# Optimization experiments

Measured on AMD Instinct MI355X. Metric: run time of the kernel, lower is better.

The kernel has to match this reference:

```python
import jax, jax.numpy as jnp
import numpy as np

B, L, D = 4, 2048, 1024
EV = 64            # event_embed_dim
EXPAND = 2
DI = EXPAND * D    # d_inner = 2048
N = 16             # d_state
K = 4              # d_conv
DT_RANK = (D + 15) // 16  # 64
EPS = 1e-5


def setup_inputs() -> dict:
    key = jax.random.key(0)
    ks = jax.random.split(key, 16)
    g = lambda k, shape, s=0.02: (jax.random.normal(k, shape, dtype=jnp.float32) * s)
    return {
        "x": jax.random.normal(ks[0], (B, L, D), dtype=jnp.float32),
        "event_emb": jax.random.normal(ks[1], (B, L, EV), dtype=jnp.float32),
        "W_in": g(ks[2], (D + EV, D)),
        "b_in": jnp.zeros((D,), jnp.float32),
        "ln_g": jnp.ones((D,), jnp.float32),
        "ln_b": jnp.zeros((D,), jnp.float32),
        "in_proj_w": g(ks[3], (D, 2 * DI)),
        "conv_w": g(ks[4], (DI, K), 0.1),
        "conv_b": jnp.zeros((DI,), jnp.float32),
        "x_proj_w": g(ks[5], (DI, DT_RANK + 2 * N)),
        "dt_proj_w": g(ks[6], (DT_RANK, DI), 0.1),
        "dt_proj_b": jnp.full((DI,), -4.6, jnp.float32),  # ~softplus^-1(0.01)
        "A_log": jnp.log(jnp.broadcast_to(jnp.arange(1, N + 1, dtype=jnp.float32), (DI, N))),
        "D_param": jnp.ones((DI,), jnp.float32),
        "out_proj_w": g(ks[7], (DI, D)),
    }


def _mamba_block(x, event_emb, W_in, b_in, ln_g, ln_b, in_proj_w, conv_w, conv_b,
                 x_proj_w, dt_proj_w, dt_proj_b, A_log, D_param, out_proj_w):
    d_conv = conv_w.shape[1]
    n_state = A_log.shape[1]
    dt_rank = dt_proj_w.shape[0]
    Lx = x.shape[1]

    aug = jnp.concatenate([x, event_emb], axis=-1) @ W_in + b_in   # [B,L,D]
    residual = aug
    mu = aug.mean(-1, keepdims=True)
    var = jnp.mean((aug - mu) ** 2, axis=-1, keepdims=True)
    h = (aug - mu) * jax.lax.rsqrt(var + EPS) * ln_g + ln_b

    xz = h @ in_proj_w                                             # [B,L,2*DI]
    xh, z = jnp.split(xz, 2, axis=-1)

    # causal depthwise conv1d (width d_conv)
    xp = jnp.pad(xh, ((0, 0), (d_conv - 1, 0), (0, 0)))
    xc = conv_b
    for k in range(d_conv):
        xc = xc + conv_w[:, k] * xp[:, k:k + Lx, :]
    xc = jax.nn.silu(xc)                                           # [B,L,DI]

    dbl = xc @ x_proj_w                                            # [B,L,dt_rank+2N]
    dt, Bm, Cm = jnp.split(dbl, [dt_rank, dt_rank + n_state], axis=-1)
    dt = jax.nn.softplus(dt @ dt_proj_w + dt_proj_b)               # [B,L,DI]
    A = -jnp.exp(A_log)                                            # [DI,N]

    def step(hst, inp):
        dt_t, B_t, C_t, u_t = inp                                  # [B,DI],[B,N],[B,N],[B,DI]
        dA = jnp.exp(dt_t[:, :, None] * A)                         # [B,DI,N]
        dBu = (dt_t * u_t)[:, :, None] * B_t[:, None, :]           # [B,DI,N]
        hst = dA * hst + dBu
        y_t = jnp.einsum('bdn,bn->bd', hst, C_t)
        return hst, y_t

    h0 = jnp.zeros((xc.shape[0], xc.shape[2], n_state), xc.dtype)
    xs = (dt.transpose(1, 0, 2), Bm.transpose(1, 0, 2),
          Cm.transpose(1, 0, 2), xc.transpose(1, 0, 2))
    _, ys = jax.lax.scan(step, h0, xs)                             # [L,B,DI]
    y = ys.transpose(1, 0, 2) + D_param * xc
    y = y * jax.nn.silu(z)
    return residual + y @ out_proj_w                               # [B,L,D]


def reference(x, event_emb, W_in, b_in, ln_g, ln_b, in_proj_w, conv_w, conv_b,
              x_proj_w, dt_proj_w, dt_proj_b, A_log, D_param, out_proj_w):
    return _mamba_block(x, event_emb, W_in, b_in, ln_g, ln_b, in_proj_w, conv_w,
                        conv_b, x_proj_w, dt_proj_w, dt_proj_b, A_log, D_param,
                        out_proj_w)
```

## Files before the change

kernel.cpp:

```cpp
#include <hip/hip_runtime.h>
#include <cstdint>
#include <cstddef>

#define DEV __device__ __forceinline__

typedef __bf16 bf16x8 __attribute__((ext_vector_type(8)));
typedef float f32x4 __attribute__((ext_vector_type(4)));

DEV unsigned short f2bf(float f) {
  unsigned u = __builtin_bit_cast(unsigned, f);
  u += 0x7fffu + ((u >> 16) & 1u);
  return (unsigned short)(u >> 16);
}
DEV float bf2f(unsigned short h) {
  return __builtin_bit_cast(float, (unsigned)h << 16);
}

__global__ __launch_bounds__(256)
void k_concat(const float* __restrict__ x, const float* __restrict__ ev,
              unsigned short* __restrict__ Aaug) {
  int col4 = blockIdx.x * 256 + threadIdx.x;
  if (col4 >= 288) return;
  size_t row = blockIdx.y;
  float4 v = make_float4(0.f, 0.f, 0.f, 0.f);
  if (col4 < 256)      v = reinterpret_cast<const float4*>(x + row * 1024)[col4];
  else if (col4 < 272) v = reinterpret_cast<const float4*>(ev + row * 64)[col4 - 256];
  ushort4 o; o.x = f2bf(v.x); o.y = f2bf(v.y); o.z = f2bf(v.z); o.w = f2bf(v.w);
  reinterpret_cast<ushort4*>(Aaug + row * 1152)[col4] = o;
}

__global__ void k_transpose(const float* __restrict__ in, unsigned short* __restrict__ out,
                            int R, int C, int Rout, int Cout) {
  __shared__ float tile[32][33];
  int c0 = blockIdx.x * 32, r0 = blockIdx.y * 32;
  int tx = threadIdx.x, ty = threadIdx.y;
#pragma unroll
  for (int i = 0; i < 4; ++i) {
    int r = r0 + ty + i * 8, c = c0 + tx;
    tile[ty + i * 8][tx] = (r < R && c < C) ? in[(size_t)r * C + c] : 0.f;
  }
  __syncthreads();
#pragma unroll
  for (int i = 0; i < 4; ++i) {
    int c = c0 + ty + i * 8, r = r0 + tx;
    if (c < Cout && r < Rout) out[(size_t)c * Rout + r] = f2bf(tile[tx][ty + i * 8]);
  }
}

template <int BN, int EPI>
__global__ __launch_bounds__(512, 2)
void k_gemm8(const unsigned short* __restrict__ A, const unsigned short* __restrict__ Bt,
             int N, int NT, int lda, int ldb,
             float* __restrict__ outF, unsigned short* __restrict__ outB1,
             unsigned short* __restrict__ outB2,
             const float* __restrict__ bias, const float* __restrict__ resid) {
  static_assert(BN == 128 || BN == 256, "");
  constexpr int NF = BN / 64;
  constexpr int NHF = NF / 2;
  constexpr int BLOADS = BN / 128;
  constexpr int ATILE = 256 * 64;
  constexpr int BTILE = BN * 64;
  constexpr int BUFSZ = ATILE + BTILE;
  __shared__ unsigned short lds[2 * BUFSZ];

  const int tid = threadIdx.x;
  const int lane = tid & 63, w = tid >> 6;
  const int wm = w >> 2, wn = w & 3;
  const int frow = lane & 15, fk = lane >> 4;

  const int nbx = gridDim.x;
  const int nwg = nbx * gridDim.y;
  const int orig = blockIdx.y * nbx + blockIdx.x;
  const int swz = (orig & 7) * (nwg >> 3) + (orig >> 3);
  const int brow = swz / nbx, bcol = swz % nbx;
  const size_t row0 = (size_t)brow * 256, col0 = (size_t)bcol * BN;

  f32x4 acc[8][NF];
#pragma unroll
  for (int i = 0; i < 8; ++i)
#pragma unroll
    for (int j = 0; j < NF; ++j) acc[i][j] = f32x4{0.f, 0.f, 0.f, 0.f};

  bf16x8 afr[4][2], bq0[NHF][2], bq1[NHF][2];

  auto stageA = [&](int p, int tau, int half) {
    unsigned short* dst = lds + p * BUFSZ + half * 4096 + w * 512;
#pragma unroll
    for (int l = 0; l < 2; ++l) {
      int row = l * 128 + half * 64 + (tid >> 3);
      int g = (tid & 7) ^ (row & 7);
      const unsigned short* src = A + (row0 + row) * lda + tau * 64 + g * 8;
      __builtin_amdgcn_global_load_lds(src, dst + l * 8192, 16, 0, 0);
    }
  };
  auto stageB = [&](int p, int tau, int half) {
    unsigned short* dst = lds + p * BUFSZ + ATILE + half * (BTILE / 2) + w * 512;
#pragma unroll
    for (int l = 0; l < BLOADS; ++l) {
      int row = half * (BN / 2) + l * 64 + (tid >> 3);
      int g = (tid & 7) ^ (row & 7);
      const unsigned short* src = Bt + (col0 + row) * ldb + tau * 64 + g * 8;
      __builtin_amdgcn_global_load_lds(src, dst + l * 4096, 16, 0, 0);
    }
  };
  auto ldA = [&](int p, int mh) {
#pragma unroll
    for (int mi = 0; mi < 4; ++mi)
#pragma unroll
      for (int kb = 0; kb < 2; ++kb) {
        int rr = wm * 128 + mh * 64 + mi * 16 + frow;
        int gk = kb * 4 + fk;
        afr[mi][kb] = *reinterpret_cast<const bf16x8*>(
            lds + p * BUFSZ + rr * 64 + ((gk ^ (rr & 7)) * 8));
      }
  };
  auto ldB = [&](int p, int nh, bf16x8 (&bq)[NHF][2]) {
#pragma unroll
    for (int ni = 0; ni < NHF; ++ni)
#pragma unroll
      for (int kb = 0; kb < 2; ++kb) {
        int cc = wn * (BN / 4) + nh * (BN / 8) + ni * 16 + frow;
        int gk = kb * 4 + fk;
        bq[ni][kb] = *reinterpret_cast<const bf16x8*>(
            lds + p * BUFSZ + ATILE + cc * 64 + ((gk ^ (cc & 7)) * 8));
      }
  };

#define MMAQ(MH, NH, BQ)                                                          \
  do {                                                                            \
    __builtin_amdgcn_s_setprio(1);                                                \
    _Pragma("unroll") for (int mi = 0; mi < 4; ++mi)                              \
        _Pragma("unroll") for (int ni = 0; ni < NHF; ++ni)                        \
            _Pragma("unroll") for (int kb = 0; kb < 2; ++kb)                      \
                acc[(MH)*4 + mi][(NH)*NHF + ni] =                                 \
                    __builtin_amdgcn_mfma_f32_16x16x32_bf16(                      \
                        afr[mi][kb], BQ[ni][kb], acc[(MH)*4 + mi][(NH)*NHF + ni], \
                        0, 0, 0);                                                 \
    __builtin_amdgcn_s_setprio(0);                                                \
  } while (0)

#define BARC  __builtin_amdgcn_s_barrier()
#define SBAR  __builtin_amdgcn_sched_barrier(0)
#define EBAR  do { __builtin_amdgcn_s_barrier(); __builtin_amdgcn_sched_barrier(0); } while (0)
#define VMCNT_WAIT                                                     \
  do {                                                                 \
    if constexpr (BN == 256)                                           \
      asm volatile("s_waitcnt vmcnt(6)" ::: "memory");                 \
    else                                                               \
      asm volatile("s_waitcnt vmcnt(4)" ::: "memory");                 \
  } while (0)

  stageA(0, 0, 0); stageB(0, 0, 0); stageB(0, 0, 1); stageA(0, 0, 1);
  SBAR;
  stageA(1, 1, 0); stageB(1, 1, 0); stageB(1, 1, 1);
  VMCNT_WAIT;
  BARC; SBAR;

  const int niter = NT >> 1;
  for (int it = 0; it < niter; ++it) {
    int t = 2 * it;
    int t1s = t + 1;
    int t2s = (t + 2 < NT) ? t + 2 : NT - 1;
    int t3s = (t + 3 < NT) ? t + 3 : NT - 1;
    ldA(0, 0); ldB(0, 0, bq0);
    stageA(1, t1s, 1);
    BARC; MMAQ(0, 0, bq0); EBAR;
    ldB(0, 1, bq1);
    stageA(0, t2s, 0);
    BARC; MMAQ(0, 1, bq1); EBAR;
    ldA(0, 1);
    stageB(0, t2s, 0);
    BARC; MMAQ(1, 1, bq1); EBAR;
    stageB(0, t2s, 1);
    BARC; MMAQ(1, 0, bq0); VMCNT_WAIT; EBAR;
    ldA(1, 0); ldB(1, 0, bq0);
    stageA(0, t2s, 1);
    BARC; MMAQ(0, 0, bq0); EBAR;
    ldB(1, 1, bq1);
    stageA(1, t3s, 0);
    BARC; MMAQ(0, 1, bq1); EBAR;
    ldA(1, 1);
    stageB(1, t3s, 0);
    BARC; MMAQ(1, 1, bq1); EBAR;
    stageB(1, t3s, 1);
    BARC; MMAQ(1, 0, bq0); VMCNT_WAIT; EBAR;
  }

#pragma unroll
  for (int q = 0; q < 8; ++q) {
#pragma unroll
    for (int j = 0; j < NF; ++j) {
#pragma unroll
      for (int r = 0; r < 4; ++r) {
        size_t row = row0 + wm * 128 + q * 16 + fk * 4 + r;
        size_t col = col0 + wn * (BN / 4) + j * 16 + frow;
        float v = acc[q][j][r];
        if constexpr (EPI == 0) {
          outF[row * N + col] = v + bias[col];
        } else if constexpr (EPI == 1) {
          int hn = N >> 1;
          if ((int)col < hn) outB1[row * hn + col] = f2bf(v);
          else               outB2[row * hn + (col - hn)] = f2bf(v);
        } else {
          outF[row * N + col] = resid[row * N + col] + v;
        }
      }
    }
  }
#undef MMAQ
#undef BARC
#undef SBAR
#undef EBAR
#undef VMCNT_WAIT
}

template <int EPI>
__global__ __launch_bounds__(256)
void k_gemm(const unsigned short* __restrict__ A, const unsigned short* __restrict__ Bt,
            int N, int K, int lda, int ldb,
            unsigned short* __restrict__ outB1, const float* __restrict__ bias) {
  __shared__ alignas(16) unsigned short sA[128 * 64];
  __shared__ alignas(16) unsigned short sB[128 * 64];
  int tid = threadIdx.x;
  int lane = tid & 63, w = tid >> 6;
  int nbx = gridDim.x;
  int nwg = nbx * gridDim.y;
  int orig = blockIdx.y * nbx + blockIdx.x;
  int swz = (orig & 7) * (nwg >> 3) + (orig >> 3);
  int brow = swz / nbx, bcol = swz % nbx;
  size_t row0 = (size_t)brow * 128, col0 = (size_t)bcol * 128;

  int lrow_s = tid >> 3;
  int g_s = tid & 7;
  int wrow = (w >> 1) * 64, wcol = (w & 1) * 64;
  int frow = lane & 15, fk = lane >> 4;
  f32x4 acc[4][4] = {};

  for (int kt = 0; kt < K; kt += 64) {
    __syncthreads();
#pragma unroll
    for (int r = 0; r < 4; ++r) {
      int lr = r * 32 + lrow_s;
      int gs = g_s ^ (lr & 7);
      const unsigned short* srcA = A + (size_t)(row0 + lr) * lda + kt + gs * 8;
      const unsigned short* srcB = Bt + (size_t)(col0 + lr) * ldb + kt + gs * 8;
      unsigned short* dstA = sA + (r * 32 + w * 8) * 64;
      unsigned short* dstB = sB + (r * 32 + w * 8) * 64;
      __builtin_amdgcn_global_load_lds(srcA, dstA, 16, 0, 0);
      __builtin_amdgcn_global_load_lds(srcB, dstB, 16, 0, 0);
    }
    __syncthreads();
#pragma unroll
    for (int kw = 0; kw < 2; ++kw) {
      bf16x8 af[4], bfr[4];
      int gk = kw * 4 + fk;
#pragma unroll
      for (int mi = 0; mi < 4; ++mi) {
        int rr = wrow + mi * 16 + frow;
        af[mi] = *reinterpret_cast<const bf16x8*>(sA + rr * 64 + ((gk ^ (rr & 7)) * 8));
      }
#pragma unroll
      for (int ni = 0; ni < 4; ++ni) {
        int rr = wcol + ni * 16 + frow;
        bfr[ni] = *reinterpret_cast<const bf16x8*>(sB + rr * 64 + ((gk ^ (rr & 7)) * 8));
      }
#pragma unroll
      for (int mi = 0; mi < 4; ++mi)
#pragma unroll
        for (int ni = 0; ni < 4; ++ni)
          acc[mi][ni] = __builtin_amdgcn_mfma_f32_16x16x32_bf16(af[mi], bfr[ni], acc[mi][ni], 0, 0, 0);
    }
  }

#pragma unroll
  for (int mi = 0; mi < 4; ++mi) {
#pragma unroll
    for (int ni = 0; ni < 4; ++ni) {
#pragma unroll
      for (int r = 0; r < 4; ++r) {
        size_t row = row0 + wrow + mi * 16 + fk * 4 + r;
        size_t col = col0 + wcol + ni * 16 + frow;
        float v = acc[mi][ni][r];
        if constexpr (EPI == 2) {
          outB1[row * N + col] = f2bf(v);
        } else {
          float xx = v + bias[col];
          float sp = (xx > 15.f) ? xx : __logf(1.f + __expf(xx));
          outB1[row * N + col] = f2bf(sp);
        }
      }
    }
  }
}

__global__ __launch_bounds__(256)
void k_ln(const float* __restrict__ aug, const float* __restrict__ gam,
          const float* __restrict__ bet, unsigned short* __restrict__ h) {
  int tid = threadIdx.x;
  size_t row = blockIdx.x;
  float4 v = reinterpret_cast<const float4*>(aug + row * 1024)[tid];
  float s = v.x + v.y + v.z + v.w;
  float ss = v.x * v.x + v.y * v.y + v.z * v.z + v.w * v.w;
#pragma unroll
  for (int m = 32; m >= 1; m >>= 1) {
    s += __shfl_xor(s, m, 64);
    ss += __shfl_xor(ss, m, 64);
  }
  __shared__ float rb[8];
  if ((tid & 63) == 0) { rb[tid >> 6] = s; rb[4 + (tid >> 6)] = ss; }
  __syncthreads();
  float ts = rb[0] + rb[1] + rb[2] + rb[3];
  float tss = rb[4] + rb[5] + rb[6] + rb[7];
  float mu = ts * (1.f / 1024.f);
  float var = tss * (1.f / 1024.f) - mu * mu;
  float rs = rsqrtf(var + 1e-5f);
  float4 gv = reinterpret_cast<const float4*>(gam)[tid];
  float4 bv = reinterpret_cast<const float4*>(bet)[tid];
  ushort4 o;
  o.x = f2bf((v.x - mu) * rs * gv.x + bv.x);
  o.y = f2bf((v.y - mu) * rs * gv.y + bv.y);
  o.z = f2bf((v.z - mu) * rs * gv.z + bv.z);
  o.w = f2bf((v.w - mu) * rs * gv.w + bv.w);
  reinterpret_cast<ushort4*>(h + row * 1024)[tid] = o;
}

__global__ __launch_bounds__(256)
void k_conv(const unsigned short* __restrict__ xh, const float* __restrict__ cw,
            const float* __restrict__ cb, unsigned short* __restrict__ xc) {
  int d = blockIdx.x * 256 + threadIdx.x;
  int t = blockIdx.y, b = blockIdx.z;
  size_t rowb = (size_t)b * 2048;
  float acc = cb[d];
#pragma unroll
  for (int k = 0; k < 4; ++k) {
    int tt = t - 3 + k;
    if (tt >= 0) acc += cw[d * 4 + k] * bf2f(xh[(rowb + tt) * 2048 + d]);
  }
  float sg = 1.f / (1.f + __expf(-acc));
  xc[(rowb + t) * 2048 + d] = f2bf(acc * sg);
}

template <bool FINAL>
__global__ __launch_bounds__(256)
void k_scan(const unsigned short* __restrict__ dt, const unsigned short* __restrict__ xc,
            const unsigned short* __restrict__ dbl, const float* __restrict__ A_log,
            float* __restrict__ S, float* __restrict__ SD,
            const float* __restrict__ Hin, const float* __restrict__ Dp,
            const unsigned short* __restrict__ z, unsigned short* __restrict__ yg) {
  int d = blockIdx.x * 256 + threadIdx.x;
  int b = blockIdx.y, c = blockIdx.z;
  int t0 = c * 32;
  size_t hoff = (((size_t)c * 4 + b) * 2048 + d) * 16;
  float An[16], h[16];
  bool fast = true;
#pragma unroll
  for (int n = 0; n < 16; ++n) {
    An[n] = -__expf(A_log[((size_t)d << 4) + n]);
    fast = fast && (__builtin_fabsf(An[n] + (float)(n + 1)) < 1e-4f);
    h[n] = FINAL ? Hin[hoff + n] : 0.f;
  }
  float Dv = FINAL ? Dp[d] : 0.f;
  float dts = 0.f;
  __shared__ float sBC[32][32];
  if (threadIdx.x < 128) {
    int s = threadIdx.x >> 2, j8 = (threadIdx.x & 3) * 8;
    size_t rowg = (size_t)b * 2048 + t0 + s;
    uint4 raw = *reinterpret_cast<const uint4*>(dbl + rowg * 128 + 64 + j8);
    unsigned rr4[4] = {raw.x, raw.y, raw.z, raw.w};
#pragma unroll
    for (int q = 0; q < 4; ++q) {
      sBC[s][j8 + 2 * q]     = bf2f((unsigned short)(rr4[q] & 0xffffu));
      sBC[s][j8 + 2 * q + 1] = bf2f((unsigned short)(rr4[q] >> 16));
    }
  }
  __syncthreads();

  if (fast) {
    for (int si = 0; si < 32; ++si) {
      size_t rr = ((size_t)b * 2048 + t0 + si) * 2048 + d;
      float dtv = bf2f(dt[rr]);
      float uv = bf2f(xc[rr]);
      float dtu = dtv * uv;
      float y = 0.f;
      if constexpr (!FINAL) dts += dtv;
      float e1 = __expf(-dtv);
      float a = e1;
#pragma unroll
      for (int n = 0; n < 16; ++n) {
        h[n] = a * h[n] + dtu * sBC[si][n];
        if constexpr (FINAL) y += h[n] * sBC[si][16 + n];
        a *= e1;
      }
      if constexpr (FINAL) {
        float zv = bf2f(z[rr]);
        float sig = 1.f / (1.f + __expf(-zv));
        yg[rr] = f2bf((y + Dv * uv) * (zv * sig));
      }
    }
  } else {
    for (int si = 0; si < 32; ++si) {
      size_t rr = ((size_t)b * 2048 + t0 + si) * 2048 + d;
      float dtv = bf2f(dt[rr]);
      float uv = bf2f(xc[rr]);
      float dtu = dtv * uv;
      float y = 0.f;
      if constexpr (!FINAL) dts += dtv;
#pragma unroll
      for (int n = 0; n < 16; ++n) {
        float a = __expf(dtv * An[n]);
        h[n] = a * h[n] + dtu * sBC[si][n];
        if constexpr (FINAL) y += h[n] * sBC[si][16 + n];
      }
      if constexpr (FINAL) {
        float zv = bf2f(z[rr]);
        float sig = 1.f / (1.f + __expf(-zv));
        yg[rr] = f2bf((y + Dv * uv) * (zv * sig));
      }
    }
  }
  if constexpr (!FINAL) {
#pragma unroll
    for (int n = 0; n < 16; ++n) S[hoff + n] = h[n];
    SD[((size_t)c * 4 + b) * 2048 + d] = dts;
  }
}

__global__ __launch_bounds__(256)
void k_scanB(float* __restrict__ S, const float* __restrict__ SD,
             const float* __restrict__ A_log) {
  int id = blockIdx.x * 256 + threadIdx.x;
  int n = id & 15, d = (id >> 4) & 2047, b = id >> 15;
  float An = -__expf(A_log[((size_t)d << 4) + n]);
  float h = 0.f;
  for (int c = 0; c < 64; ++c) {
    size_t sdo = ((size_t)c * 4 + b) * 2048 + d;
    size_t o = sdo * 16 + n;
    float s = S[o];
    float p = __expf(An * SD[sdo]);
    S[o] = h;
    h = s + p * h;
  }
}

extern "C" void kernel_launch(void* const* d_in, const int* in_sizes, int n_in,
                              void* d_out, int out_size, void* d_ws, size_t ws_size,
                              hipStream_t stream) {
  const float* x       = (const float*)d_in[0];
  const float* ev      = (const float*)d_in[1];
  const float* W_in    = (const float*)d_in[2];
  const float* b_in    = (const float*)d_in[3];
  const float* ln_g    = (const float*)d_in[4];
  const float* ln_b    = (const float*)d_in[5];
  const float* in_proj = (const float*)d_in[6];
  const float* conv_w  = (const float*)d_in[7];
  const float* conv_b  = (const float*)d_in[8];
  const float* x_proj  = (const float*)d_in[9];
  const float* dt_proj = (const float*)d_in[10];
  const float* dt_b    = (const float*)d_in[11];
  const float* A_log   = (const float*)d_in[12];
  const float* D_par   = (const float*)d_in[13];
  const float* out_w   = (const float*)d_in[14];
  float* out = (float*)d_out;

  char* ws = (char*)d_ws;
  size_t off = 0;
  auto alloc = [&](size_t bytes) {
    char* p = ws + off;
    off = (off + bytes + 255) & ~(size_t)255;
    return p;
  };
  float* aug            = (float*)alloc(8192ull * 1024 * 4);
  unsigned short* dtfb  = (unsigned short*)alloc(8192ull * 2048 * 2);
  unsigned short* Aaug  = (unsigned short*)alloc(8192ull * 1152 * 2);
  unsigned short* WinT  = (unsigned short*)alloc(1024ull * 1152 * 2);
  unsigned short* ipT   = (unsigned short*)alloc(4096ull * 1024 * 2);
  unsigned short* xpT   = (unsigned short*)alloc(128ull * 2048 * 2);
  unsigned short* dpT   = (unsigned short*)alloc(2048ull * 64 * 2);
  unsigned short* opT   = (unsigned short*)alloc(1024ull * 2048 * 2);
  unsigned short* xh    = (unsigned short*)alloc(8192ull * 2048 * 2);
  unsigned short* zb    = (unsigned short*)alloc(8192ull * 2048 * 2);
  unsigned short* xcb   = (unsigned short*)alloc(8192ull * 2048 * 2);
  unsigned short* dbl   = (unsigned short*)alloc(8192ull * 128 * 2);
  float* Sb = (float*)alloc(64ull * 4 * 2048 * 16 * 4);
  float* SD = (float*)alloc(64ull * 4 * 2048 * 4);
  unsigned short* hb = Aaug;
  unsigned short* yg = xh;

  k_concat<<<dim3(2, 8192), 256, 0, stream>>>(x, ev, Aaug);
  k_transpose<<<dim3(32, 36), dim3(32, 8), 0, stream>>>(W_in, WinT, 1088, 1024, 1152, 1024);
  k_transpose<<<dim3(128, 32), dim3(32, 8), 0, stream>>>(in_proj, ipT, 1024, 4096, 1024, 4096);
  k_transpose<<<dim3(4, 64), dim3(32, 8), 0, stream>>>(x_proj, xpT, 2048, 96, 2048, 128);
  k_transpose<<<dim3(64, 2), dim3(32, 8), 0, stream>>>(dt_proj, dpT, 64, 2048, 64, 2048);
  k_transpose<<<dim3(32, 64), dim3(32, 8), 0, stream>>>(out_w, opT, 2048, 1024, 2048, 1024);

  k_gemm8<128, 0><<<dim3(8, 32), 512, 0, stream>>>(Aaug, WinT, 1024, 18, 1152, 1152,
                                                   aug, nullptr, nullptr, b_in, nullptr);
  k_ln<<<dim3(8192), 256, 0, stream>>>(aug, ln_g, ln_b, hb);
  k_gemm8<256, 1><<<dim3(16, 32), 512, 0, stream>>>(hb, ipT, 4096, 16, 1024, 1024,
                                                    nullptr, xh, zb, nullptr, nullptr);
  k_conv<<<dim3(8, 2048, 4), 256, 0, stream>>>(xh, conv_w, conv_b, xcb);
  k_gemm<2><<<dim3(1, 64), 256, 0, stream>>>(xcb, xpT, 128, 2048, 2048, 2048, dbl, nullptr);
  k_gemm<3><<<dim3(16, 64), 256, 0, stream>>>(dbl, dpT, 2048, 64, 128, 64, dtfb, dt_b);
  k_scan<false><<<dim3(8, 4, 64), 256, 0, stream>>>(dtfb, xcb, dbl, A_log, Sb, SD,
                                                    nullptr, nullptr, nullptr, nullptr);
  k_scanB<<<dim3(512), 256, 0, stream>>>(Sb, SD, A_log);
  k_scan<true><<<dim3(8, 4, 64), 256, 0, stream>>>(dtfb, xcb, dbl, A_log, nullptr, nullptr,
                                                   Sb, D_par, zb, yg);
  k_gemm8<128, 4><<<dim3(8, 32), 512, 0, stream>>>(yg, opT, 1024, 32, 2048, 2048,
                                                   out, nullptr, nullptr, nullptr, aug);
}
```

Before: 412.9 us.

## Switch GEMMs to 32x32 MFMA, add multi-tile persistent blocks, split scan exponent chain

The GEMM kernel moves from 16x16x32 to 32x32x16 bf16 MFMA fragments with f32x16 accumulators, which changes the LDS fragment loads and the epilogue layout. A new MT template parameter lets one workgroup process two M tiles back to back without draining the pipeline, with an in-loop epilogue that writes results and clears the accumulators. The in_proj GEMM uses MT=2 on half the grid. Separately, the scan's serial a*=e1 power chain is replaced by precomputed powers to shorten the dependency chain. Together these aim to raise MFMA throughput and ILP, at the cost of register pressure and a different output access pattern.

```diff
diff --git a/kernel.cpp b/kernel.cpp
--- a/kernel.cpp
+++ b/kernel.cpp
@@ -6,6 +6,7 @@
 
 typedef __bf16 bf16x8 __attribute__((ext_vector_type(8)));
 typedef float f32x4 __attribute__((ext_vector_type(4)));
+typedef float f32x16 __attribute__((ext_vector_type(16)));
 
 DEV unsigned short f2bf(float f) {
   unsigned u = __builtin_bit_cast(unsigned, f);
@@ -47,7 +48,7 @@
   }
 }
 
-template <int BN, int EPI>
+template <int BN, int MT, int EPI>
 __global__ __launch_bounds__(512, 2)
 void k_gemm8(const unsigned short* __restrict__ A, const unsigned short* __restrict__ Bt,
              int N, int NT, int lda, int ldb,
@@ -55,8 +56,8 @@
              unsigned short* __restrict__ outB2,
              const float* __restrict__ bias, const float* __restrict__ resid) {
   static_assert(BN == 128 || BN == 256, "");
-  constexpr int NF = BN / 64;
-  constexpr int NHF = NF / 2;
+  constexpr int NC = BN / 128;
+  constexpr int BQN = (BN == 256) ? 4 : 2;
   constexpr int BLOADS = BN / 128;
   constexpr int ATILE = 256 * 64;
   constexpr int BTILE = BN * 64;
@@ -66,77 +67,85 @@
   const int tid = threadIdx.x;
   const int lane = tid & 63, w = tid >> 6;
   const int wm = w >> 2, wn = w & 3;
-  const int frow = lane & 15, fk = lane >> 4;
+  const int ln31 = lane & 31, lk = lane >> 5;
 
   const int nbx = gridDim.x;
   const int nwg = nbx * gridDim.y;
   const int orig = blockIdx.y * nbx + blockIdx.x;
   const int swz = (orig & 7) * (nwg >> 3) + (orig >> 3);
   const int brow = swz / nbx, bcol = swz % nbx;
-  const size_t row0 = (size_t)brow * 256, col0 = (size_t)bcol * BN;
-
-  f32x4 acc[8][NF];
-#pragma unroll
-  for (int i = 0; i < 8; ++i)
-#pragma unroll
-    for (int j = 0; j < NF; ++j) acc[i][j] = f32x4{0.f, 0.f, 0.f, 0.f};
-
-  bf16x8 afr[4][2], bq0[NHF][2], bq1[NHF][2];
+  const size_t rowBase = (size_t)brow * (256 * MT);
+  const size_t col0 = (size_t)bcol * BN;
+  const int TT = MT * NT;
+
+  f32x16 acc[4][NC];
+#pragma unroll
+  for (int i = 0; i < 4; ++i)
+#pragma unroll
+    for (int j = 0; j < NC; ++j)
+#pragma unroll
+      for (int r = 0; r < 16; ++r) acc[i][j][r] = 0.f;
+
+  bf16x8 afr[2][4], bq0[BQN], bq1[BQN];
 
   auto stageA = [&](int p, int tau, int half) {
+    int tm = (MT > 1 && tau >= NT) ? 1 : 0;
+    int kt = tau - tm * NT;
     unsigned short* dst = lds + p * BUFSZ + half * 4096 + w * 512;
 #pragma unroll
     for (int l = 0; l < 2; ++l) {
       int row = l * 128 + half * 64 + (tid >> 3);
       int g = (tid & 7) ^ (row & 7);
-      const unsigned short* src = A + (row0 + row) * lda + tau * 64 + g * 8;
+      const unsigned short* src = A + (rowBase + tm * 256 + row) * lda + kt * 64 + g * 8;
       __builtin_amdgcn_global_load_lds(src, dst + l * 8192, 16, 0, 0);
     }
   };
   auto stageB = [&](int p, int tau, int half) {
+    int tm = (MT > 1 && tau >= NT) ? 1 : 0;
+    int kt = tau - tm * NT;
     unsigned short* dst = lds + p * BUFSZ + ATILE + half * (BTILE / 2) + w * 512;
 #pragma unroll
     for (int l = 0; l < BLOADS; ++l) {
       int row = half * (BN / 2) + l * 64 + (tid >> 3);
       int g = (tid & 7) ^ (row & 7);
-      const unsigned short* src = Bt + (col0 + row) * ldb + tau * 64 + g * 8;
+      const unsigned short* src = Bt + (col0 + row) * ldb + kt * 64 + g * 8;
       __builtin_amdgcn_global_load_lds(src, dst + l * 4096, 16, 0, 0);
     }
   };
   auto ldA = [&](int p, int mh) {
 #pragma unroll
-    for (int mi = 0; mi < 4; ++mi)
-#pragma unroll
-      for (int kb = 0; kb < 2; ++kb) {
-        int rr = wm * 128 + mh * 64 + mi * 16 + frow;
-        int gk = kb * 4 + fk;
-        afr[mi][kb] = *reinterpret_cast<const bf16x8*>(
+    for (int mf = 0; mf < 2; ++mf)
+#pragma unroll
+      for (int ks = 0; ks < 4; ++ks) {
+        int rr = wm * 128 + mh * 64 + mf * 32 + ln31;
+        int gk = ks * 2 + lk;
+        afr[mf][ks] = *reinterpret_cast<const bf16x8*>(
             lds + p * BUFSZ + rr * 64 + ((gk ^ (rr & 7)) * 8));
       }
   };
-  auto ldB = [&](int p, int nh, bf16x8 (&bq)[NHF][2]) {
-#pragma unroll
-    for (int ni = 0; ni < NHF; ++ni)
-#pragma unroll
-      for (int kb = 0; kb < 2; ++kb) {
-        int cc = wn * (BN / 4) + nh * (BN / 8) + ni * 16 + frow;
-        int gk = kb * 4 + fk;
-        bq[ni][kb] = *reinterpret_cast<const bf16x8*>(
-            lds + p * BUFSZ + ATILE + cc * 64 + ((gk ^ (cc & 7)) * 8));
-      }
+  auto ldB = [&](int p, int nh, bf16x8 (&bq)[BQN]) {
+#pragma unroll
+    for (int q = 0; q < BQN; ++q) {
+      int nf = (BN == 256) ? nh : 0;
+      int ks = (BN == 256) ? q : (nh * 2 + q);
+      int cc = wn * (BN / 4) + nf * 32 + ln31;
+      int gk = ks * 2 + lk;
+      bq[q] = *reinterpret_cast<const bf16x8*>(
+          lds + p * BUFSZ + ATILE + cc * 64 + ((gk ^ (cc & 7)) * 8));
+    }
   };
 
-#define MMAQ(MH, NH, BQ)                                                          \
-  do {                                                                            \
-    __builtin_amdgcn_s_setprio(1);                                                \
-    _Pragma("unroll") for (int mi = 0; mi < 4; ++mi)                              \
-        _Pragma("unroll") for (int ni = 0; ni < NHF; ++ni)                        \
-            _Pragma("unroll") for (int kb = 0; kb < 2; ++kb)                      \
-                acc[(MH)*4 + mi][(NH)*NHF + ni] =                                 \
-                    __builtin_amdgcn_mfma_f32_16x16x32_bf16(                      \
-                        afr[mi][kb], BQ[ni][kb], acc[(MH)*4 + mi][(NH)*NHF + ni], \
-                        0, 0, 0);                                                 \
-    __builtin_amdgcn_s_setprio(0);                                                \
+#define MMAQ(MH, NH, BQ)                                                           \
+  do {                                                                             \
+    __builtin_amdgcn_s_setprio(1);                                                 \
+    _Pragma("unroll") for (int mf = 0; mf < 2; ++mf)                               \
+        _Pragma("unroll") for (int q = 0; q < BQN; ++q) {                          \
+      constexpr int nfi = (BN == 256) ? (NH) : 0;                                  \
+      acc[(MH)*2 + mf][nfi] = __builtin_amdgcn_mfma_f32_32x32x16_bf16(             \
+          afr[mf][(BN == 256) ? q : ((NH)*2 + q)], BQ[q], acc[(MH)*2 + mf][nfi],   \
+          0, 0, 0);                                                                \
+    }                                                                              \
+    __builtin_amdgcn_s_setprio(0);                                                 \
   } while (0)
 
 #define BARC  __builtin_amdgcn_s_barrier()
@@ -150,18 +159,45 @@
       asm volatile("s_waitcnt vmcnt(4)" ::: "memory");                 \
   } while (0)
 
+  auto epilogue = [&](int tm) {
+    size_t tRow0 = rowBase + (size_t)tm * 256;
+#pragma unroll
+    for (int mf = 0; mf < 4; ++mf) {
+#pragma unroll
+      for (int nf = 0; nf < NC; ++nf) {
+#pragma unroll
+        for (int r = 0; r < 16; ++r) {
+          size_t row = tRow0 + wm * 128 + mf * 32 + (r & 3) + 8 * (r >> 2) + 4 * lk;
+          size_t col = col0 + wn * (BN / 4) + nf * 32 + ln31;
+          float v = acc[mf][nf][r];
+          if constexpr (EPI == 0) {
+            outF[row * N + col] = v + bias[col];
+          } else if constexpr (EPI == 1) {
+            int hn = N >> 1;
+            if ((int)col < hn) outB1[row * hn + col] = f2bf(v);
+            else               outB2[row * hn + (col - hn)] = f2bf(v);
+          } else {
+            outF[row * N + col] = resid[row * N + col] + v;
+          }
+          acc[mf][nf][r] = 0.f;
+        }
+      }
+    }
+  };
+
   stageA(0, 0, 0); stageB(0, 0, 0); stageB(0, 0, 1); stageA(0, 0, 1);
   SBAR;
   stageA(1, 1, 0); stageB(1, 1, 0); stageB(1, 1, 1);
   VMCNT_WAIT;
   BARC; SBAR;
 
-  const int niter = NT >> 1;
+  int kcnt = 0, tmdone = 0;
+  const int niter = TT >> 1;
   for (int it = 0; it < niter; ++it) {
     int t = 2 * it;
     int t1s = t + 1;
-    int t2s = (t + 2 < NT) ? t + 2 : NT - 1;
-    int t3s = (t + 3 < NT) ? t + 3 : NT - 1;
+    int t2s = (t + 2 < TT) ? t + 2 : TT - 1;
+    int t3s = (t + 3 < TT) ? t + 3 : TT - 1;
     ldA(0, 0); ldB(0, 0, bq0);
     stageA(1, t1s, 1);
     BARC; MMAQ(0, 0, bq0); EBAR;
@@ -184,28 +220,8 @@
     BARC; MMAQ(1, 1, bq1); EBAR;
     stageB(1, t3s, 1);
     BARC; MMAQ(1, 0, bq0); VMCNT_WAIT; EBAR;
-  }
-
-#pragma unroll
-  for (int q = 0; q < 8; ++q) {
-#pragma unroll
-    for (int j = 0; j < NF; ++j) {
-#pragma unroll
-      for (int r = 0; r < 4; ++r) {
-        size_t row = row0 + wm * 128 + q * 16 + fk * 4 + r;
-        size_t col = col0 + wn * (BN / 4) + j * 16 + frow;
-        float v = acc[q][j][r];
-        if constexpr (EPI == 0) {
-          outF[row * N + col] = v + bias[col];
-        } else if constexpr (EPI == 1) {
-          int hn = N >> 1;
-          if ((int)col < hn) outB1[row * hn + col] = f2bf(v);
-          else               outB2[row * hn + (col - hn)] = f2bf(v);
-        } else {
-          outF[row * N + col] = resid[row * N + col] + v;
-        }
-      }
-    }
+    kcnt += 2;
+    if (kcnt == NT) { epilogue(tmdone); ++tmdone; kcnt = 0; }
   }
 #undef MMAQ
 #undef BARC
@@ -384,12 +400,16 @@
       float y = 0.f;
       if constexpr (!FINAL) dts += dtv;
       float e1 = __expf(-dtv);
-      float a = e1;
+      float e2 = e1 * e1;
+      float e3 = e2 * e1, e4 = e2 * e2;
+      float e8 = e4 * e4, e12 = e8 * e4;
+      float base[4] = {e1, e2, e3, e4};
+      float mul[4] = {1.f, e4, e8, e12};
 #pragma unroll
       for (int n = 0; n < 16; ++n) {
+        float a = base[n & 3] * mul[n >> 2];
         h[n] = a * h[n] + dtu * sBC[si][n];
         if constexpr (FINAL) y += h[n] * sBC[si][16 + n];
-        a *= e1;
       }
       if constexpr (FINAL) {
         float zv = bf2f(z[rr]);
@@ -493,11 +513,11 @@
   k_transpose<<<dim3(64, 2), dim3(32, 8), 0, stream>>>(dt_proj, dpT, 64, 2048, 64, 2048);
   k_transpose<<<dim3(32, 64), dim3(32, 8), 0, stream>>>(out_w, opT, 2048, 1024, 2048, 1024);
 
-  k_gemm8<128, 0><<<dim3(8, 32), 512, 0, stream>>>(Aaug, WinT, 1024, 18, 1152, 1152,
-                                                   aug, nullptr, nullptr, b_in, nullptr);
+  k_gemm8<128, 1, 0><<<dim3(8, 32), 512, 0, stream>>>(Aaug, WinT, 1024, 18, 1152, 1152,
+                                                      aug, nullptr, nullptr, b_in, nullptr);
   k_ln<<<dim3(8192), 256, 0, stream>>>(aug, ln_g, ln_b, hb);
-  k_gemm8<256, 1><<<dim3(16, 32), 512, 0, stream>>>(hb, ipT, 4096, 16, 1024, 1024,
-                                                    nullptr, xh, zb, nullptr, nullptr);
+  k_gemm8<256, 2, 1><<<dim3(16, 16), 512, 0, stream>>>(hb, ipT, 4096, 16, 1024, 1024,
+                                                       nullptr, xh, zb, nullptr, nullptr);
   k_conv<<<dim3(8, 2048, 4), 256, 0, stream>>>(xh, conv_w, conv_b, xcb);
   k_gemm<2><<<dim3(1, 64), 256, 0, stream>>>(xcb, xpT, 128, 2048, 2048, 2048, dbl, nullptr);
   k_gemm<3><<<dim3(16, 64), 256, 0, stream>>>(dbl, dpT, 2048, 64, 128, 64, dtfb, dt_b);
@@ -506,6 +526,6 @@
   k_scanB<<<dim3(512), 256, 0, stream>>>(Sb, SD, A_log);
   k_scan<true><<<dim3(8, 4, 64), 256, 0, stream>>>(dtfb, xcb, dbl, A_log, nullptr, nullptr,
                                                    Sb, D_par, zb, yg);
-  k_gemm8<128, 4><<<dim3(8, 32), 512, 0, stream>>>(yg, opT, 1024, 32, 2048, 2048,
-                                                   out, nullptr, nullptr, nullptr, aug);
-}
+  k_gemm8<128, 1, 4><<<dim3(8, 32), 512, 0, stream>>>(yg, opT, 1024, 32, 2048, 2048,
+                                                      out, nullptr, nullptr, nullptr, aug);
+}
```

Result: slower. 474.4 us (+14.9%).

## Hoist GEMM address math, vectorize conv, break scan decay dependency chain

Applied to the files above, without the earlier changes.

The GEMM kernel now precomputes its global source offsets and swizzled LDS fragment addresses once, instead of recomputing them per stage, and relaxes launch bounds from 2 to 1 block per CU so more registers are available. The depthwise conv kernel now has each thread handle 8 channels with vector loads and stores, launched one block per row. The scan's fast path computes the decay powers from a few base products rather than a serial multiply chain, shortening the dependency chain. The risks are lower occupancy in the GEMM and higher register use in conv.

```diff
diff --git a/kernel.cpp b/kernel.cpp
--- a/kernel.cpp
+++ b/kernel.cpp
@@ -48,7 +48,7 @@
 }
 
 template <int BN, int EPI>
-__global__ __launch_bounds__(512, 2)
+__global__ __launch_bounds__(512, 1)
 void k_gemm8(const unsigned short* __restrict__ A, const unsigned short* __restrict__ Bt,
              int N, int NT, int lda, int ldb,
              float* __restrict__ outF, unsigned short* __restrict__ outB1,
@@ -83,47 +83,61 @@
 
   bf16x8 afr[4][2], bq0[NHF][2], bq1[NHF][2];
 
+  const int srow = tid >> 3;
+  const int g8 = ((tid & 7) ^ (srow & 7)) * 8;
+  const size_t offA_h0l0 = (row0 + 0 * 128 + 0 * 64 + srow) * (size_t)lda + g8;
+  const size_t offA_h0l1 = (row0 + 1 * 128 + 0 * 64 + srow) * (size_t)lda + g8;
+  const size_t offA_h1l0 = (row0 + 0 * 128 + 1 * 64 + srow) * (size_t)lda + g8;
+  const size_t offA_h1l1 = (row0 + 1 * 128 + 1 * 64 + srow) * (size_t)lda + g8;
+  const size_t offB_h0l0 = (col0 + 0 * (BN / 2) + 0 * 64 + srow) * (size_t)ldb + g8;
+  const size_t offB_h1l0 = (col0 + 1 * (BN / 2) + 0 * 64 + srow) * (size_t)ldb + g8;
+  const size_t offB_h0l1 = (BLOADS == 2) ? ((col0 + 0 * (BN / 2) + 1 * 64 + srow) * (size_t)ldb + g8) : 0;
+  const size_t offB_h1l1 = (BLOADS == 2) ? ((col0 + 1 * (BN / 2) + 1 * 64 + srow) * (size_t)ldb + g8) : 0;
+
+  char* ldsb = reinterpret_cast<char*>(lds);
+  const int fr7 = frow & 7;
+  const int slot0 = (fk ^ fr7) * 16;
+  const int slot1 = ((4 + fk) ^ fr7) * 16;
+  const int abase0 = (wm * 128 + frow) * 128 + slot0;
+  const int abase1 = (wm * 128 + frow) * 128 + slot1;
+  const int bbase0 = (wn * (BN / 4) + frow) * 128 + slot0 + ATILE * 2;
+  const int bbase1 = (wn * (BN / 4) + frow) * 128 + slot1 + ATILE * 2;
+
   auto stageA = [&](int p, int tau, int half) {
+    const size_t kadd = (size_t)tau * 64;
+    const unsigned short* s0 = A + (half ? offA_h1l0 : offA_h0l0) + kadd;
+    const unsigned short* s1 = A + (half ? offA_h1l1 : offA_h0l1) + kadd;
     unsigned short* dst = lds + p * BUFSZ + half * 4096 + w * 512;
-#pragma unroll
-    for (int l = 0; l < 2; ++l) {
-      int row = l * 128 + half * 64 + (tid >> 3);
-      int g = (tid & 7) ^ (row & 7);
-      const unsigned short* src = A + (row0 + row) * lda + tau * 64 + g * 8;
-      __builtin_amdgcn_global_load_lds(src, dst + l * 8192, 16, 0, 0);
-    }
+    __builtin_amdgcn_global_load_lds(s0, dst, 16, 0, 0);
+    __builtin_amdgcn_global_load_lds(s1, dst + 8192, 16, 0, 0);
   };
   auto stageB = [&](int p, int tau, int half) {
+    const size_t kadd = (size_t)tau * 64;
     unsigned short* dst = lds + p * BUFSZ + ATILE + half * (BTILE / 2) + w * 512;
-#pragma unroll
-    for (int l = 0; l < BLOADS; ++l) {
-      int row = half * (BN / 2) + l * 64 + (tid >> 3);
-      int g = (tid & 7) ^ (row & 7);
-      const unsigned short* src = Bt + (col0 + row) * ldb + tau * 64 + g * 8;
-      __builtin_amdgcn_global_load_lds(src, dst + l * 4096, 16, 0, 0);
+    const unsigned short* s0 = Bt + (half ? offB_h1l0 : offB_h0l0) + kadd;
+    __builtin_amdgcn_global_load_lds(s0, dst, 16, 0, 0);
+    if constexpr (BLOADS == 2) {
+      const unsigned short* s1 = Bt + (half ? offB_h1l1 : offB_h0l1) + kadd;
+      __builtin_amdgcn_global_load_lds(s1, dst + 4096, 16, 0, 0);
     }
   };
   auto ldA = [&](int p, int mh) {
-#pragma unroll
-    for (int mi = 0; mi < 4; ++mi)
-#pragma unroll
-      for (int kb = 0; kb < 2; ++kb) {
-        int rr = wm * 128 + mh * 64 + mi * 16 + frow;
-        int gk = kb * 4 + fk;
-        afr[mi][kb] = *reinterpret_cast<const bf16x8*>(
-            lds + p * BUFSZ + rr * 64 + ((gk ^ (rr & 7)) * 8));
-      }
+    const int pb = p * (BUFSZ * 2);
+#pragma unroll
+    for (int mi = 0; mi < 4; ++mi) {
+      const int off = pb + (mh * 64 + mi * 16) * 128;
+      afr[mi][0] = *reinterpret_cast<const bf16x8*>(ldsb + abase0 + off);
+      afr[mi][1] = *reinterpret_cast<const bf16x8*>(ldsb + abase1 + off);
+    }
   };
   auto ldB = [&](int p, int nh, bf16x8 (&bq)[NHF][2]) {
-#pragma unroll
-    for (int ni = 0; ni < NHF; ++ni)
-#pragma unroll
-      for (int kb = 0; kb < 2; ++kb) {
-        int cc = wn * (BN / 4) + nh * (BN / 8) + ni * 16 + frow;
-        int gk = kb * 4 + fk;
-        bq[ni][kb] = *reinterpret_cast<const bf16x8*>(
-            lds + p * BUFSZ + ATILE + cc * 64 + ((gk ^ (cc & 7)) * 8));
-      }
+    const int pb = p * (BUFSZ * 2);
+#pragma unroll
+    for (int ni = 0; ni < NHF; ++ni) {
+      const int off = pb + (nh * (BN / 8) + ni * 16) * 128;
+      bq[ni][0] = *reinterpret_cast<const bf16x8*>(ldsb + bbase0 + off);
+      bq[ni][1] = *reinterpret_cast<const bf16x8*>(ldsb + bbase1 + off);
+    }
   };
 
 #define MMAQ(MH, NH, BQ)                                                          \
@@ -327,17 +341,45 @@
 __global__ __launch_bounds__(256)
 void k_conv(const unsigned short* __restrict__ xh, const float* __restrict__ cw,
             const float* __restrict__ cb, unsigned short* __restrict__ xc) {
-  int d = blockIdx.x * 256 + threadIdx.x;
-  int t = blockIdx.y, b = blockIdx.z;
-  size_t rowb = (size_t)b * 2048;
-  float acc = cb[d];
+  size_t row = blockIdx.x;
+  int t = (int)(row & 2047);
+  size_t rowb = row - t;
+  int d = threadIdx.x * 8;
+  float acc[8];
+  {
+    float4 c0 = *reinterpret_cast<const float4*>(cb + d);
+    float4 c1 = *reinterpret_cast<const float4*>(cb + d + 4);
+    acc[0] = c0.x; acc[1] = c0.y; acc[2] = c0.z; acc[3] = c0.w;
+    acc[4] = c1.x; acc[5] = c1.y; acc[6] = c1.z; acc[7] = c1.w;
+  }
+  float wv[8][4];
+#pragma unroll
+  for (int j = 0; j < 8; ++j) {
+    float4 cj = *reinterpret_cast<const float4*>(cw + (size_t)(d + j) * 4);
+    wv[j][0] = cj.x; wv[j][1] = cj.y; wv[j][2] = cj.z; wv[j][3] = cj.w;
+  }
 #pragma unroll
   for (int k = 0; k < 4; ++k) {
     int tt = t - 3 + k;
-    if (tt >= 0) acc += cw[d * 4 + k] * bf2f(xh[(rowb + tt) * 2048 + d]);
-  }
-  float sg = 1.f / (1.f + __expf(-acc));
-  xc[(rowb + t) * 2048 + d] = f2bf(acc * sg);
+    if (tt >= 0) {
+      ushort4 va = reinterpret_cast<const ushort4*>(xh + (rowb + tt) * 2048 + d)[0];
+      ushort4 vb = reinterpret_cast<const ushort4*>(xh + (rowb + tt) * 2048 + d)[1];
+      unsigned short e[8] = {va.x, va.y, va.z, va.w, vb.x, vb.y, vb.z, vb.w};
+#pragma unroll
+      for (int j = 0; j < 8; ++j) acc[j] += wv[j][k] * bf2f(e[j]);
+    }
+  }
+  ushort4 o0, o1;
+  unsigned short* op = &o0.x;
+#pragma unroll
+  for (int j = 0; j < 8; ++j) {
+    float sg = 1.f / (1.f + __expf(-acc[j]));
+    unsigned short r = f2bf(acc[j] * sg);
+    if (j < 4) (&o0.x)[j] = r; else (&o1.x)[j - 4] = r;
+  }
+  (void)op;
+  reinterpret_cast<ushort4*>(xc + row * 2048 + d)[0] = o0;
+  reinterpret_cast<ushort4*>(xc + row * 2048 + d)[1] = o1;
 }
 
 template <bool FINAL>
@@ -384,12 +426,16 @@
       float y = 0.f;
       if constexpr (!FINAL) dts += dtv;
       float e1 = __expf(-dtv);
-      float a = e1;
+      float e2 = e1 * e1;
+      float e3 = e2 * e1, e4 = e2 * e2;
+      float e8 = e4 * e4, e12 = e8 * e4;
+      float base[4] = {e1, e2, e3, e4};
+      float mul[4] = {1.f, e4, e8, e12};
 #pragma unroll
       for (int n = 0; n < 16; ++n) {
+        float a = base[n & 3] * mul[n >> 2];
         h[n] = a * h[n] + dtu * sBC[si][n];
         if constexpr (FINAL) y += h[n] * sBC[si][16 + n];
-        a *= e1;
       }
       if constexpr (FINAL) {
         float zv = bf2f(z[rr]);
@@ -498,7 +544,7 @@
   k_ln<<<dim3(8192), 256, 0, stream>>>(aug, ln_g, ln_b, hb);
   k_gemm8<256, 1><<<dim3(16, 32), 512, 0, stream>>>(hb, ipT, 4096, 16, 1024, 1024,
                                                     nullptr, xh, zb, nullptr, nullptr);
-  k_conv<<<dim3(8, 2048, 4), 256, 0, stream>>>(xh, conv_w, conv_b, xcb);
+  k_conv<<<dim3(8192), 256, 0, stream>>>(xh, conv_w, conv_b, xcb);
   k_gemm<2><<<dim3(1, 64), 256, 0, stream>>>(xcb, xpT, 128, 2048, 2048, 2048, dbl, nullptr);
   k_gemm<3><<<dim3(16, 64), 256, 0, stream>>>(dbl, dpT, 2048, 64, 128, 64, dtfb, dt_b);
   k_scan<false><<<dim3(8, 4, 64), 256, 0, stream>>>(dtfb, xcb, dbl, A_log, Sb, SD,
```

Result: no change. 407.3 us (-1.3%).
